# Performance work log

Hardware: AMD Instinct MI355X
Metric: run time of the kernel (lower is better)

Reference implementation:

```python
import jax, jax.numpy as jnp
import numpy as np

N = 50000      # nodes
E = 800000     # edges
IN = 128       # in_channels
HID = 32       # hidden_channels (per head)
HEADS = 4
OUT = 128      # out_channels
NEG_SLOPE = 0.2  # PyG GATConv leaky relu slope


def setup_inputs() -> dict:
    key = jax.random.key(0)
    ks = jax.random.split(key, 10)
    x = jax.random.normal(ks[0], (N, IN), dtype=jnp.float32)
    edge_index = jax.random.randint(ks[1], (2, E), 0, N, dtype=jnp.int32)
    s1 = 1.0 / np.sqrt(IN)
    s2 = 1.0 / np.sqrt(HEADS * HID)
    W1 = jax.random.normal(ks[2], (IN, HEADS * HID), dtype=jnp.float32) * s1
    a_src1 = jax.random.normal(ks[3], (HEADS, HID), dtype=jnp.float32) * s1
    a_dst1 = jax.random.normal(ks[4], (HEADS, HID), dtype=jnp.float32) * s1
    b1 = jnp.zeros((HEADS * HID,), dtype=jnp.float32)
    W2 = jax.random.normal(ks[5], (HEADS * HID, OUT), dtype=jnp.float32) * s2
    a_src2 = jax.random.normal(ks[6], (1, OUT), dtype=jnp.float32) * s2
    a_dst2 = jax.random.normal(ks[7], (1, OUT), dtype=jnp.float32) * s2
    b2 = jnp.zeros((OUT,), dtype=jnp.float32)
    return {"x": x, "edge_index": edge_index, "W1": W1, "a_src1": a_src1,
            "a_dst1": a_dst1, "b1": b1, "W2": W2, "a_src2": a_src2,
            "a_dst2": a_dst2, "b2": b2}


def _gat_layer(x, src, dst, W, a_src, a_dst, bias, heads, out_c, concat, n):
    # dense projection then reshape to [N, H, C]
    h = (x @ W).reshape(n, heads, out_c)
    # per-node attention halves: [N, H]
    alpha_src = jnp.einsum('nhc,hc->nh', h, a_src)
    alpha_dst = jnp.einsum('nhc,hc->nh', h, a_dst)
    # per-edge logits, leaky relu (slope 0.2 as in PyG)
    logits = jax.nn.leaky_relu(alpha_src[src] + alpha_dst[dst], NEG_SLOPE)  # [E', H]
    # segment softmax over incoming edges of each destination node
    m = jax.ops.segment_max(logits, dst, num_segments=n)          # [N, H]
    e = jnp.exp(logits - m[dst])                                   # [E', H]
    denom = jax.ops.segment_sum(e, dst, num_segments=n)           # [N, H]
    alpha = e / (denom[dst] + 1e-16)                               # [E', H]
    # weighted scatter-aggregate of source features
    out = jax.ops.segment_sum(alpha[:, :, None] * h[src], dst, num_segments=n)  # [N, H, C]
    if concat:
        out = out.reshape(n, heads * out_c)
    else:
        out = out.mean(axis=1)
    return out + bias


def reference(x, edge_index, W1, a_src1, a_dst1, b1, W2, a_src2, a_dst2, b2):
    n = x.shape[0]
    # PyG GATConv adds self-loops by default
    loop = jnp.arange(n, dtype=edge_index.dtype)
    src = jnp.concatenate([edge_index[0], loop])
    dst = jnp.concatenate([edge_index[1], loop])
    h = _gat_layer(x, src, dst, W1, a_src1, a_dst1, b1, HEADS, HID, True, n)
    h = jax.nn.elu(h)
    # dropout is identity in eval mode
    out = _gat_layer(h, src, dst, W2, a_src2, a_dst2, b2, 1, OUT, False, n)
    return jax.nn.elu(out)
```

## Files before the change

kernel.cpp:

```cpp
#include <hip/hip_runtime.h>
#include <hip/hip_bf16.h>


typedef _Float16 half2_t __attribute__((ext_vector_type(2)));
typedef _Float16 half4_t __attribute__((ext_vector_type(4)));
typedef _Float16 f16x8 __attribute__((ext_vector_type(8)));
typedef float f32x4 __attribute__((ext_vector_type(4)));

#define NBLK1 128
#define SORT_CAP 6144

static __device__ __forceinline__ float leaky02(float x) {
    return x > 0.f ? x : 0.2f * x;
}
static __device__ __forceinline__ float elu1(float x) {
    return x > 0.f ? x : __expf(x) - 1.f;
}


__global__ __launch_bounds__(256) void prep_kernel(
    const int* __restrict__ dst, int* __restrict__ g_cnt, int E, int chunk,
    const float* __restrict__ W1, const float* __restrict__ W2,
    _Float16* __restrict__ Wt1, _Float16* __restrict__ Wt2, int nbkt) {
    int b = blockIdx.x;
    int t = threadIdx.x;
    if (b < NBLK1) {
        __shared__ int h[256];
        h[t] = 0;
        __syncthreads();
        int lo = b * chunk, hi = min(E, lo + chunk);
        for (int i = lo + t; i < hi; i += 256) atomicAdd(&h[dst[i] >> 8], 1);
        __syncthreads();
        if (t < nbkt) g_cnt[t * NBLK1 + b] = h[t];
    } else {
        int idx = (b - NBLK1) * 256 + t;
        int which = idx >> 14;
        int r = idx & 16383;
        int nc = r >> 7, k = r & 127;
        if (which == 0)
            Wt1[(size_t)nc * 128 + k] = (_Float16)W1[(size_t)k * 128 + nc];
        else
            Wt2[(size_t)nc * 128 + k] = (_Float16)W2[(size_t)k * 128 + nc];
    }
}

__global__ void scan_tile_kernel(const int* __restrict__ in, int* __restrict__ out,
                                 int* __restrict__ sums, int n) {
    __shared__ int sdata[256];
    int t = threadIdx.x;
    int base = blockIdx.x * 2048 + t * 8;
    int v[8];
    int run = 0;
#pragma unroll
    for (int i = 0; i < 8; ++i) {
        int idx = base + i;
        int x = (idx < n) ? in[idx] : 0;
        run += x;
        v[i] = run;
    }
    sdata[t] = run;
    __syncthreads();
    for (int off = 1; off < 256; off <<= 1) {
        int u = (t >= off) ? sdata[t - off] : 0;
        __syncthreads();
        sdata[t] += u;
        __syncthreads();
    }
    int excl = sdata[t] - run;
#pragma unroll
    for (int i = 0; i < 8; ++i) {
        int idx = base + i;
        if (idx < n) out[idx] = v[i] + excl;
    }
    if (t == 0) sums[blockIdx.x] = sdata[255];
}

__global__ void scan_sums_kernel(int* __restrict__ sums, int nb) {
    int t = threadIdx.x;
    int orig = (t < nb) ? sums[t] : 0;
    int v = orig;
#pragma unroll
    for (int off = 1; off < 64; off <<= 1) {
        int u = __shfl_up(v, off, 64);
        if (t >= off) v += u;
    }
    if (t < nb) sums[t] = v - orig;
}

__global__ void offs_kernel(const int* __restrict__ incl, const int* __restrict__ sums,
                            int* __restrict__ offs, int ncnt) {
    int i = blockIdx.x * blockDim.x + threadIdx.x;
    if (i <= ncnt) offs[i] = (i == 0) ? 0 : incl[i - 1] + sums[(i - 1) >> 11];
}


__global__ __launch_bounds__(256) void gemm1_fused_kernel(
    const float* __restrict__ X, const _Float16* __restrict__ Wt,
    _Float16* __restrict__ H16, int nrows, const int* __restrict__ src,
    const int* __restrict__ dst, const int* __restrict__ offs,
    int* __restrict__ binned, int E, int chunk, int nGemm, int nbkt) {
    int b = blockIdx.x;
    int t = threadIdx.x;
    if (b < nGemm) {
        int wave = t >> 6, lane = t & 63;
        int m = lane & 15, q = lane >> 4;
        int arow = b * 64 + wave * 16 + m;
        bool rowok = arow < nrows;
        const float* xr = X + (size_t)arow * 128;
        f16x8 afrag[4];
#pragma unroll
        for (int s = 0; s < 4; ++s) {
            float4 v0 = make_float4(0.f, 0.f, 0.f, 0.f);
            float4 v1 = make_float4(0.f, 0.f, 0.f, 0.f);
            if (rowok) {
                v0 = *(const float4*)(xr + s * 32 + q * 8);
                v1 = *(const float4*)(xr + s * 32 + q * 8 + 4);
            }
            f16x8 a;
            a[0] = (_Float16)v0.x; a[1] = (_Float16)v0.y;
            a[2] = (_Float16)v0.z; a[3] = (_Float16)v0.w;
            a[4] = (_Float16)v1.x; a[5] = (_Float16)v1.y;
            a[6] = (_Float16)v1.z; a[7] = (_Float16)v1.w;
            afrag[s] = a;
        }
#pragma unroll
        for (int c = 0; c < 8; ++c) {
            f32x4 acc = {0.f, 0.f, 0.f, 0.f};
#pragma unroll
            for (int s = 0; s < 4; ++s) {
                f16x8 bfrag = *(const f16x8*)(Wt + (size_t)(c * 16 + m) * 128 + s * 32 + q * 8);
                acc = __builtin_amdgcn_mfma_f32_16x16x32_f16(afrag[s], bfrag, acc, 0, 0, 0);
            }
#pragma unroll
            for (int r = 0; r < 4; ++r) {
                int orow = b * 64 + wave * 16 + q * 4 + r;
                if (orow < nrows)
                    H16[(size_t)orow * 128 + c * 16 + m] = (_Float16)acc[r];
            }
        }
    } else {
        __shared__ int cur[256];
        int sb = b - nGemm;
        if (t < nbkt) cur[t] = offs[t * NBLK1 + sb];
        __syncthreads();
        int lo = sb * chunk, hi = min(E, lo + chunk);
        for (int i = lo + t; i < hi; i += 256) {
            int d = dst[i];
            int s = src[i];
            int p = atomicAdd(&cur[d >> 8], 1);
            binned[p] = ((d & 255) << 16) | s;
        }
    }
}


__global__ __launch_bounds__(256) void sort_alpha1_kernel(
    const int* __restrict__ binned, const int* __restrict__ offs,
    int* __restrict__ row_ptr, int* __restrict__ csr, int n, int nbkt,
    const _Float16* __restrict__ H16, const float* __restrict__ a_src,
    const float* __restrict__ a_dst, float* __restrict__ asrc_out,
    float* __restrict__ adst_out) {
    int b = blockIdx.x;
    int t = threadIdx.x;
    if (b < nbkt) {
        __shared__ int sorted[SORT_CAP];
        __shared__ int sdata[256];
        __shared__ int cur[256];
        int estart = offs[b * NBLK1];
        int eend = offs[(b + 1) * NBLK1];
        int node0 = b * 256;
        int nloc = min(256, n - node0);
        cur[t] = (t < nloc) ? 1 : 0;
        __syncthreads();
        for (int i = estart + t; i < eend; i += 256)
            atomicAdd(&cur[(binned[i] >> 16) & 255], 1);
        __syncthreads();
        int my = cur[t];
        sdata[t] = my;
        __syncthreads();
        for (int off = 1; off < 256; off <<= 1) {
            int u = (t >= off) ? sdata[t - off] : 0;
            __syncthreads();
            sdata[t] += u;
            __syncthreads();
        }
        int excl = sdata[t] - my;
        int total = sdata[255];
        int csr_base = estart + node0;
        if (node0 + t <= n) row_ptr[node0 + t] = csr_base + excl;
        if (t == 0 && node0 + 256 <= n) row_ptr[node0 + 256] = csr_base + total;
        if (t < nloc) {
            if (excl < SORT_CAP) sorted[excl] = node0 + t;
            else csr[csr_base + excl] = node0 + t;
            cur[t] = excl + 1;
        } else {
            cur[t] = 0;
        }
        __syncthreads();
        for (int i = estart + t; i < eend; i += 256) {
            int v = binned[i];
            int p = atomicAdd(&cur[(v >> 16) & 255], 1);
            int sv = v & 0xffff;
            if (p < SORT_CAP) sorted[p] = sv;
            else csr[csr_base + p] = sv;
        }
        __syncthreads();
        int lim = min(total, SORT_CAP);
        for (int j = t; j < lim; j += 256) csr[csr_base + j] = sorted[j];
    } else {
        int node = (b - nbkt) * 4 + (t >> 6);
        int lane = t & 63;
        if (node >= n) return;
        int c = lane * 2;
        half2_t hv = *(const half2_t*)(H16 + (size_t)node * 128 + c);
        float2 as = *(const float2*)(a_src + c);
        float2 ad = *(const float2*)(a_dst + c);
        float hx = (float)hv.x, hy = (float)hv.y;
        float ps = hx * as.x + hy * as.y;
        float pd = hx * ad.x + hy * ad.y;
#pragma unroll
        for (int off = 1; off <= 8; off <<= 1) {
            ps += __shfl_xor(ps, off, 64);
            pd += __shfl_xor(pd, off, 64);
        }
        if ((lane & 15) == 0) {
            int h = lane >> 4;
            asrc_out[node * 4 + h] = ps;
            adst_out[node * 4 + h] = pd;
        }
    }
}

__global__ __launch_bounds__(256) void gemm2_mfma_kernel(
    const _Float16* __restrict__ A16, const _Float16* __restrict__ Wt,
    _Float16* __restrict__ H16, int nrows) {
    int b = blockIdx.x;
    int t = threadIdx.x;
    int wave = t >> 6, lane = t & 63;
    int m = lane & 15, q = lane >> 4;
    int arow = b * 64 + wave * 16 + m;
    bool rowok = arow < nrows;
    const _Float16* ar = A16 + (size_t)arow * 128;
    f16x8 afrag[4];
#pragma unroll
    for (int s = 0; s < 4; ++s) {
        f16x8 a = {};
        if (rowok) a = *(const f16x8*)(ar + s * 32 + q * 8);
        afrag[s] = a;
    }
#pragma unroll
    for (int c = 0; c < 8; ++c) {
        f32x4 acc = {0.f, 0.f, 0.f, 0.f};
#pragma unroll
        for (int s = 0; s < 4; ++s) {
            f16x8 bfrag = *(const f16x8*)(Wt + (size_t)(c * 16 + m) * 128 + s * 32 + q * 8);
            acc = __builtin_amdgcn_mfma_f32_16x16x32_f16(afrag[s], bfrag, acc, 0, 0, 0);
        }
#pragma unroll
        for (int r = 0; r < 4; ++r) {
            int orow = b * 64 + wave * 16 + q * 4 + r;
            if (orow < nrows)
                H16[(size_t)orow * 128 + c * 16 + m] = (_Float16)acc[r];
        }
    }
}

__global__ void alpha2_kernel(const _Float16* __restrict__ H16, const float* __restrict__ a_src,
                              const float* __restrict__ a_dst, float* __restrict__ asrc_out,
                              float* __restrict__ adst_out, int n) {
    int wave = (blockIdx.x * blockDim.x + threadIdx.x) >> 6;
    int lane = threadIdx.x & 63;
    if (wave >= n) return;
    int c = lane * 2;
    half2_t hv = *(const half2_t*)(H16 + (size_t)wave * 128 + c);
    float2 as = *(const float2*)(a_src + c);
    float2 ad = *(const float2*)(a_dst + c);
    float hx = (float)hv.x, hy = (float)hv.y;
    float ps = hx * as.x + hy * as.y;
    float pd = hx * ad.x + hy * ad.y;
#pragma unroll
    for (int off = 1; off <= 32; off <<= 1) {
        ps += __shfl_xor(ps, off, 64);
        pd += __shfl_xor(pd, off, 64);
    }
    if (lane == 0) {
        asrc_out[wave] = ps;
        adst_out[wave] = pd;
    }
}


__global__ __launch_bounds__(256) void agg1_kernel(
    const _Float16* __restrict__ H16, const float* __restrict__ asrc,
    const float* __restrict__ adst, const int* __restrict__ row_ptr,
    const int* __restrict__ csr, const float* __restrict__ bias,
    _Float16* __restrict__ out16, int n) {
    int wid = (blockIdx.x * blockDim.x + threadIdx.x) >> 6;
    int lane = threadIdx.x & 63;
    int node = wid * 4 + (lane >> 4);
    if (node >= n) return;
    int sub = lane & 15;
    int c = sub * 8;
    int h = sub >> 2;
    float adh = adst[node * 4 + h];
    float4 bv0 = *(const float4*)(bias + c);
    float4 bv1 = *(const float4*)(bias + c + 4);
    int e0 = row_ptr[node];
    int e1 = row_ptr[node + 1];
    float den = 0.f;
    float a[8];
#pragma unroll
    for (int k = 0; k < 8; ++k) a[k] = 0.f;
    int e = e0;
    for (; e + 8 <= e1; e += 8) {
        int s[8];
#pragma unroll
        for (int j = 0; j < 8; ++j) s[j] = csr[e + j];
        float l[8];
        f16x8 g[8];
#pragma unroll
        for (int j = 0; j < 8; ++j) {
            l[j] = asrc[s[j] * 4 + h];
            g[j] = *(const f16x8*)(H16 + (size_t)s[j] * 128 + c);
        }
#pragma unroll
        for (int j = 0; j < 8; ++j) {
            float w = __expf(leaky02(l[j] + adh));
            den += w;
#pragma unroll
            for (int k = 0; k < 8; ++k) a[k] += w * (float)g[j][k];
        }
    }
    for (; e < e1; ++e) {
        int s = csr[e];
        float w = __expf(leaky02(asrc[s * 4 + h] + adh));
        f16x8 g = *(const f16x8*)(H16 + (size_t)s * 128 + c);
        den += w;
#pragma unroll
        for (int k = 0; k < 8; ++k) a[k] += w * (float)g[k];
    }
    float inv = 1.f / (den + 1e-16f);
    f16x8 o;
    o[0] = (_Float16)elu1(a[0] * inv + bv0.x);
    o[1] = (_Float16)elu1(a[1] * inv + bv0.y);
    o[2] = (_Float16)elu1(a[2] * inv + bv0.z);
    o[3] = (_Float16)elu1(a[3] * inv + bv0.w);
    o[4] = (_Float16)elu1(a[4] * inv + bv1.x);
    o[5] = (_Float16)elu1(a[5] * inv + bv1.y);
    o[6] = (_Float16)elu1(a[6] * inv + bv1.z);
    o[7] = (_Float16)elu1(a[7] * inv + bv1.w);
    *(f16x8*)(out16 + (size_t)node * 128 + c) = o;
}

__global__ __launch_bounds__(256) void agg2_kernel(
    const _Float16* __restrict__ H16, const float* __restrict__ asrc,
    const float* __restrict__ adst, const int* __restrict__ row_ptr,
    const int* __restrict__ csr, const float* __restrict__ bias,
    float* __restrict__ out, int n) {
    int wid = (blockIdx.x * blockDim.x + threadIdx.x) >> 6;
    int lane = threadIdx.x & 63;
    int node = wid * 4 + (lane >> 4);
    if (node >= n) return;
    int sub = lane & 15;
    int c = sub * 8;
    float adh = adst[node];
    float4 bv0 = *(const float4*)(bias + c);
    float4 bv1 = *(const float4*)(bias + c + 4);
    int e0 = row_ptr[node];
    int e1 = row_ptr[node + 1];
    float den = 0.f;
    float a[8];
#pragma unroll
    for (int k = 0; k < 8; ++k) a[k] = 0.f;
    int e = e0;
    for (; e + 8 <= e1; e += 8) {
        int s[8];
#pragma unroll
        for (int j = 0; j < 8; ++j) s[j] = csr[e + j];
        float l[8];
        f16x8 g[8];
#pragma unroll
        for (int j = 0; j < 8; ++j) {
            l[j] = asrc[s[j]];
            g[j] = *(const f16x8*)(H16 + (size_t)s[j] * 128 + c);
        }
#pragma unroll
        for (int j = 0; j < 8; ++j) {
            float w = __expf(leaky02(l[j] + adh));
            den += w;
#pragma unroll
            for (int k = 0; k < 8; ++k) a[k] += w * (float)g[j][k];
        }
    }
    for (; e < e1; ++e) {
        int s = csr[e];
        float w = __expf(leaky02(asrc[s] + adh));
        f16x8 g = *(const f16x8*)(H16 + (size_t)s * 128 + c);
        den += w;
#pragma unroll
        for (int k = 0; k < 8; ++k) a[k] += w * (float)g[k];
    }
    float inv = 1.f / (den + 1e-16f);
    float4 o0, o1;
    o0.x = elu1(a[0] * inv + bv0.x);
    o0.y = elu1(a[1] * inv + bv0.y);
    o0.z = elu1(a[2] * inv + bv0.z);
    o0.w = elu1(a[3] * inv + bv0.w);
    o1.x = elu1(a[4] * inv + bv1.x);
    o1.y = elu1(a[5] * inv + bv1.y);
    o1.z = elu1(a[6] * inv + bv1.z);
    o1.w = elu1(a[7] * inv + bv1.w);
    *(float4*)(out + (size_t)node * 128 + c) = o0;
    *(float4*)(out + (size_t)node * 128 + c + 4) = o1;
}


extern "C" void kernel_launch(void* const* d_in, const int* in_sizes, int n_in,
                              void* d_out, int out_size, void* d_ws, size_t ws_size,
                              hipStream_t stream) {
    const float* x       = (const float*)d_in[0];
    const int*   eidx    = (const int*)d_in[1];
    const float* W1      = (const float*)d_in[2];
    const float* a_src1  = (const float*)d_in[3];
    const float* a_dst1  = (const float*)d_in[4];
    const float* b1      = (const float*)d_in[5];
    const float* W2      = (const float*)d_in[6];
    const float* a_src2  = (const float*)d_in[7];
    const float* a_dst2  = (const float*)d_in[8];
    const float* b2      = (const float*)d_in[9];
    float* out = (float*)d_out;

    const int N = in_sizes[0] / 128;
    const int E = in_sizes[1] / 2;
    const int* src = eidx;
    const int* dst = eidx + E;

    const int nbkt = (N + 255) >> 8;
    const int ncnt = nbkt * NBLK1;
    const int chunk = (E + NBLK1 - 1) / NBLK1;
    const int ntiles = (ncnt + 2047) / 2048;

    char* w = (char*)d_ws;
    _Float16* bufH16 = (_Float16*)w; w += (size_t)N * 128 * sizeof(_Float16);
    _Float16* Wt1    = (_Float16*)w; w += (size_t)128 * 128 * sizeof(_Float16);
    _Float16* Wt2    = (_Float16*)w; w += (size_t)128 * 128 * sizeof(_Float16);
    float* asrc = (float*)w;   w += (size_t)N * 4 * sizeof(float);
    float* adst = (float*)w;   w += (size_t)N * 4 * sizeof(float);
    int* g_cnt   = (int*)w;    w += (size_t)ncnt * sizeof(int);
    int* incl    = (int*)w;    w += (size_t)ncnt * sizeof(int);
    int* offs    = (int*)w;    w += (size_t)(ncnt + 1) * sizeof(int);
    int* sums    = (int*)w;    w += 64 * sizeof(int);
    int* row_ptr = (int*)w;    w += (size_t)(N + 1) * sizeof(int);
    int* binned  = (int*)w;    w += (size_t)E * sizeof(int);
    int* csr     = (int*)w;    w += (size_t)(E + N) * sizeof(int);
    _Float16* bufA16 = (_Float16*)d_out;

    dim3 b256(256);
    const int nGemm = (N + 63) / 64;
    const int nAlpha = (N + 3) / 4;
    dim3 gAgg((((N + 3) / 4) + 3) / 4);

    hipLaunchKernelGGL(prep_kernel, dim3(NBLK1 + 128), b256, 0, stream, dst, g_cnt, E, chunk,
                       W1, W2, Wt1, Wt2, nbkt);
    hipLaunchKernelGGL(scan_tile_kernel, dim3(ntiles), b256, 0, stream, g_cnt, incl, sums, ncnt);
    hipLaunchKernelGGL(scan_sums_kernel, dim3(1), dim3(64), 0, stream, sums, ntiles);
    hipLaunchKernelGGL(offs_kernel, dim3((ncnt + 256) / 256 + 1), b256, 0, stream, incl, sums,
                       offs, ncnt);

    hipLaunchKernelGGL(gemm1_fused_kernel, dim3(nGemm + NBLK1), b256, 0, stream, x, Wt1,
                       bufH16, N, src, dst, offs, binned, E, chunk, nGemm, nbkt);
    hipLaunchKernelGGL(sort_alpha1_kernel, dim3(nbkt + nAlpha), b256, 0, stream, binned, offs,
                       row_ptr, csr, N, nbkt, bufH16, a_src1, a_dst1, asrc, adst);
    hipLaunchKernelGGL(agg1_kernel, gAgg, b256, 0, stream, bufH16, asrc, adst, row_ptr, csr, b1,
                       bufA16, N);

    hipLaunchKernelGGL(gemm2_mfma_kernel, dim3(nGemm), b256, 0, stream, bufA16, Wt2, bufH16, N);
    hipLaunchKernelGGL(alpha2_kernel, dim3(nAlpha), b256, 0, stream, bufH16, a_src2, a_dst2,
                       asrc, adst, N);
    hipLaunchKernelGGL(agg2_kernel, gAgg, b256, 0, stream, bufH16, asrc, adst, row_ptr, csr, b2,
                       out, N);
}
```

Before: 253.0 us.

## Fuse alpha2 into gemm2, collapse scan into one kernel, two nodes per agg wave

```diff
diff --git a/kernel.cpp b/kernel.cpp
--- a/kernel.cpp
+++ b/kernel.cpp
@@ -44,53 +44,29 @@
     }
 }
 
-__global__ void scan_tile_kernel(const int* __restrict__ in, int* __restrict__ out,
-                                 int* __restrict__ sums, int n) {
-    __shared__ int sdata[256];
+
+__global__ __launch_bounds__(256) void scan_one_kernel(const int* __restrict__ g_cnt,
+                                                       int* __restrict__ offs, int ncnt) {
+    __shared__ int ssum[256];
     int t = threadIdx.x;
-    int base = blockIdx.x * 2048 + t * 8;
-    int v[8];
-    int run = 0;
-#pragma unroll
-    for (int i = 0; i < 8; ++i) {
-        int idx = base + i;
-        int x = (idx < n) ? in[idx] : 0;
-        run += x;
-        v[i] = run;
-    }
-    sdata[t] = run;
+    int per = (ncnt + 255) / 256;
+    int lo = t * per, hi = min(ncnt, lo + per);
+    int s = 0;
+    for (int i = lo; i < hi; ++i) s += g_cnt[i];
+    ssum[t] = s;
     __syncthreads();
     for (int off = 1; off < 256; off <<= 1) {
-        int u = (t >= off) ? sdata[t - off] : 0;
-        __syncthreads();
-        sdata[t] += u;
-        __syncthreads();
-    }
-    int excl = sdata[t] - run;
-#pragma unroll
-    for (int i = 0; i < 8; ++i) {
-        int idx = base + i;
-        if (idx < n) out[idx] = v[i] + excl;
-    }
-    if (t == 0) sums[blockIdx.x] = sdata[255];
-}
-
-__global__ void scan_sums_kernel(int* __restrict__ sums, int nb) {
-    int t = threadIdx.x;
-    int orig = (t < nb) ? sums[t] : 0;
-    int v = orig;
-#pragma unroll
-    for (int off = 1; off < 64; off <<= 1) {
-        int u = __shfl_up(v, off, 64);
-        if (t >= off) v += u;
-    }
-    if (t < nb) sums[t] = v - orig;
-}
-
-__global__ void offs_kernel(const int* __restrict__ incl, const int* __restrict__ sums,
-                            int* __restrict__ offs, int ncnt) {
-    int i = blockIdx.x * blockDim.x + threadIdx.x;
-    if (i <= ncnt) offs[i] = (i == 0) ? 0 : incl[i - 1] + sums[(i - 1) >> 11];
+        int u = (t >= off) ? ssum[t - off] : 0;
+        __syncthreads();
+        ssum[t] += u;
+        __syncthreads();
+    }
+    int run = ssum[t] - s;
+    for (int i = lo; i < hi; ++i) {
+        offs[i] = run;
+        run += g_cnt[i];
+    }
+    if (t == 255) offs[ncnt] = run;
 }
 
 
@@ -231,9 +207,12 @@
     }
 }
 
-__global__ __launch_bounds__(256) void gemm2_mfma_kernel(
+
+__global__ __launch_bounds__(256) void gemm2_fused_kernel(
     const _Float16* __restrict__ A16, const _Float16* __restrict__ Wt,
-    _Float16* __restrict__ H16, int nrows) {
+    _Float16* __restrict__ H16, int nrows, const float* __restrict__ a_src,
+    const float* __restrict__ a_dst, float* __restrict__ asrc_out,
+    float* __restrict__ adst_out) {
     int b = blockIdx.x;
     int t = threadIdx.x;
     int wave = t >> 6, lane = t & 63;
@@ -248,6 +227,8 @@
         if (rowok) a = *(const f16x8*)(ar + s * 32 + q * 8);
         afrag[s] = a;
     }
+    float ps[4] = {0.f, 0.f, 0.f, 0.f};
+    float pd[4] = {0.f, 0.f, 0.f, 0.f};
 #pragma unroll
     for (int c = 0; c < 8; ++c) {
         f32x4 acc = {0.f, 0.f, 0.f, 0.f};
@@ -256,162 +237,168 @@
             f16x8 bfrag = *(const f16x8*)(Wt + (size_t)(c * 16 + m) * 128 + s * 32 + q * 8);
             acc = __builtin_amdgcn_mfma_f32_16x16x32_f16(afrag[s], bfrag, acc, 0, 0, 0);
         }
+        float asv = a_src[c * 16 + m];
+        float adv = a_dst[c * 16 + m];
 #pragma unroll
         for (int r = 0; r < 4; ++r) {
+            ps[r] += acc[r] * asv;
+            pd[r] += acc[r] * adv;
             int orow = b * 64 + wave * 16 + q * 4 + r;
             if (orow < nrows)
                 H16[(size_t)orow * 128 + c * 16 + m] = (_Float16)acc[r];
         }
     }
-}
-
-__global__ void alpha2_kernel(const _Float16* __restrict__ H16, const float* __restrict__ a_src,
-                              const float* __restrict__ a_dst, float* __restrict__ asrc_out,
-                              float* __restrict__ adst_out, int n) {
-    int wave = (blockIdx.x * blockDim.x + threadIdx.x) >> 6;
-    int lane = threadIdx.x & 63;
-    if (wave >= n) return;
-    int c = lane * 2;
-    half2_t hv = *(const half2_t*)(H16 + (size_t)wave * 128 + c);
-    float2 as = *(const float2*)(a_src + c);
-    float2 ad = *(const float2*)(a_dst + c);
-    float hx = (float)hv.x, hy = (float)hv.y;
-    float ps = hx * as.x + hy * as.y;
-    float pd = hx * ad.x + hy * ad.y;
-#pragma unroll
-    for (int off = 1; off <= 32; off <<= 1) {
-        ps += __shfl_xor(ps, off, 64);
-        pd += __shfl_xor(pd, off, 64);
-    }
-    if (lane == 0) {
-        asrc_out[wave] = ps;
-        adst_out[wave] = pd;
-    }
-}
-
-
-__global__ __launch_bounds__(256) void agg1_kernel(
+#pragma unroll
+    for (int r = 0; r < 4; ++r) {
+        float v = ps[r], u = pd[r];
+#pragma unroll
+        for (int off = 1; off <= 8; off <<= 1) {
+            v += __shfl_xor(v, off, 64);
+            u += __shfl_xor(u, off, 64);
+        }
+        ps[r] = v; pd[r] = u;
+    }
+    if (m == 0) {
+#pragma unroll
+        for (int r = 0; r < 4; ++r) {
+            int row = b * 64 + wave * 16 + q * 4 + r;
+            if (row < nrows) {
+                asrc_out[row] = ps[r];
+                adst_out[row] = pd[r];
+            }
+        }
+    }
+}
+
+
+__global__ __launch_bounds__(256, 6) void agg1_kernel(
     const _Float16* __restrict__ H16, const float* __restrict__ asrc,
     const float* __restrict__ adst, const int* __restrict__ row_ptr,
     const int* __restrict__ csr, const float* __restrict__ bias,
     _Float16* __restrict__ out16, int n) {
     int wid = (blockIdx.x * blockDim.x + threadIdx.x) >> 6;
     int lane = threadIdx.x & 63;
-    int node = wid * 4 + (lane >> 4);
-    if (node >= n) return;
     int sub = lane & 15;
     int c = sub * 8;
     int h = sub >> 2;
-    float adh = adst[node * 4 + h];
     float4 bv0 = *(const float4*)(bias + c);
     float4 bv1 = *(const float4*)(bias + c + 4);
-    int e0 = row_ptr[node];
-    int e1 = row_ptr[node + 1];
-    float den = 0.f;
-    float a[8];
-#pragma unroll
-    for (int k = 0; k < 8; ++k) a[k] = 0.f;
-    int e = e0;
-    for (; e + 8 <= e1; e += 8) {
-        int s[8];
-#pragma unroll
-        for (int j = 0; j < 8; ++j) s[j] = csr[e + j];
-        float l[8];
-        f16x8 g[8];
-#pragma unroll
-        for (int j = 0; j < 8; ++j) {
-            l[j] = asrc[s[j] * 4 + h];
-            g[j] = *(const f16x8*)(H16 + (size_t)s[j] * 128 + c);
-        }
-#pragma unroll
-        for (int j = 0; j < 8; ++j) {
-            float w = __expf(leaky02(l[j] + adh));
+#pragma unroll
+    for (int qq = 0; qq < 2; ++qq) {
+        int node = wid * 8 + qq * 4 + (lane >> 4);
+        if (node >= n) continue;
+        float adh = adst[node * 4 + h];
+        int e0 = row_ptr[node];
+        int e1 = row_ptr[node + 1];
+        float den = 0.f;
+        float a[8];
+#pragma unroll
+        for (int k = 0; k < 8; ++k) a[k] = 0.f;
+        int e = e0;
+        for (; e + 8 <= e1; e += 8) {
+            int s[8];
+#pragma unroll
+            for (int j = 0; j < 8; ++j) s[j] = csr[e + j];
+            float l[8];
+            f16x8 g[8];
+#pragma unroll
+            for (int j = 0; j < 8; ++j) {
+                l[j] = asrc[s[j] * 4 + h];
+                g[j] = *(const f16x8*)(H16 + (size_t)s[j] * 128 + c);
+            }
+#pragma unroll
+            for (int j = 0; j < 8; ++j) {
+                float w = __expf(leaky02(l[j] + adh));
+                den += w;
+#pragma unroll
+                for (int k = 0; k < 8; ++k) a[k] += w * (float)g[j][k];
+            }
+        }
+        for (; e < e1; ++e) {
+            int s = csr[e];
+            float w = __expf(leaky02(asrc[s * 4 + h] + adh));
+            f16x8 g = *(const f16x8*)(H16 + (size_t)s * 128 + c);
             den += w;
 #pragma unroll
-            for (int k = 0; k < 8; ++k) a[k] += w * (float)g[j][k];
-        }
-    }
-    for (; e < e1; ++e) {
-        int s = csr[e];
-        float w = __expf(leaky02(asrc[s * 4 + h] + adh));
-        f16x8 g = *(const f16x8*)(H16 + (size_t)s * 128 + c);
-        den += w;
-#pragma unroll
-        for (int k = 0; k < 8; ++k) a[k] += w * (float)g[k];
-    }
-    float inv = 1.f / (den + 1e-16f);
-    f16x8 o;
-    o[0] = (_Float16)elu1(a[0] * inv + bv0.x);
-    o[1] = (_Float16)elu1(a[1] * inv + bv0.y);
-    o[2] = (_Float16)elu1(a[2] * inv + bv0.z);
-    o[3] = (_Float16)elu1(a[3] * inv + bv0.w);
-    o[4] = (_Float16)elu1(a[4] * inv + bv1.x);
-    o[5] = (_Float16)elu1(a[5] * inv + bv1.y);
-    o[6] = (_Float16)elu1(a[6] * inv + bv1.z);
-    o[7] = (_Float16)elu1(a[7] * inv + bv1.w);
-    *(f16x8*)(out16 + (size_t)node * 128 + c) = o;
-}
-
-__global__ __launch_bounds__(256) void agg2_kernel(
+            for (int k = 0; k < 8; ++k) a[k] += w * (float)g[k];
+        }
+        float inv = 1.f / (den + 1e-16f);
+        f16x8 o;
+        o[0] = (_Float16)elu1(a[0] * inv + bv0.x);
+        o[1] = (_Float16)elu1(a[1] * inv + bv0.y);
+        o[2] = (_Float16)elu1(a[2] * inv + bv0.z);
+        o[3] = (_Float16)elu1(a[3] * inv + bv0.w);
+        o[4] = (_Float16)elu1(a[4] * inv + bv1.x);
+        o[5] = (_Float16)elu1(a[5] * inv + bv1.y);
+        o[6] = (_Float16)elu1(a[6] * inv + bv1.z);
+        o[7] = (_Float16)elu1(a[7] * inv + bv1.w);
+        *(f16x8*)(out16 + (size_t)node * 128 + c) = o;
+    }
+}
+
+__global__ __launch_bounds__(256, 6) void agg2_kernel(
     const _Float16* __restrict__ H16, const float* __restrict__ asrc,
     const float* __restrict__ adst, const int* __restrict__ row_ptr,
     const int* __restrict__ csr, const float* __restrict__ bias,
     float* __restrict__ out, int n) {
     int wid = (blockIdx.x * blockDim.x + threadIdx.x) >> 6;
     int lane = threadIdx.x & 63;
-    int node = wid * 4 + (lane >> 4);
-    if (node >= n) return;
     int sub = lane & 15;
     int c = sub * 8;
-    float adh = adst[node];
     float4 bv0 = *(const float4*)(bias + c);
     float4 bv1 = *(const float4*)(bias + c + 4);
-    int e0 = row_ptr[node];
-    int e1 = row_ptr[node + 1];
-    float den = 0.f;
-    float a[8];
-#pragma unroll
-    for (int k = 0; k < 8; ++k) a[k] = 0.f;
-    int e = e0;
-    for (; e + 8 <= e1; e += 8) {
-        int s[8];
-#pragma unroll
-        for (int j = 0; j < 8; ++j) s[j] = csr[e + j];
-        float l[8];
-        f16x8 g[8];
-#pragma unroll
-        for (int j = 0; j < 8; ++j) {
-            l[j] = asrc[s[j]];
-            g[j] = *(const f16x8*)(H16 + (size_t)s[j] * 128 + c);
-        }
-#pragma unroll
-        for (int j = 0; j < 8; ++j) {
-            float w = __expf(leaky02(l[j] + adh));
+#pragma unroll
+    for (int qq = 0; qq < 2; ++qq) {
+        int node = wid * 8 + qq * 4 + (lane >> 4);
+        if (node >= n) continue;
+        float adh = adst[node];
+        int e0 = row_ptr[node];
+        int e1 = row_ptr[node + 1];
+        float den = 0.f;
+        float a[8];
+#pragma unroll
+        for (int k = 0; k < 8; ++k) a[k] = 0.f;
+        int e = e0;
+        for (; e + 8 <= e1; e += 8) {
+            int s[8];
+#pragma unroll
+            for (int j = 0; j < 8; ++j) s[j] = csr[e + j];
+            float l[8];
+            f16x8 g[8];
+#pragma unroll
+            for (int j = 0; j < 8; ++j) {
+                l[j] = asrc[s[j]];
+                g[j] = *(const f16x8*)(H16 + (size_t)s[j] * 128 + c);
+            }
+#pragma unroll
+            for (int j = 0; j < 8; ++j) {
+                float w = __expf(leaky02(l[j] + adh));
+                den += w;
+#pragma unroll
+                for (int k = 0; k < 8; ++k) a[k] += w * (float)g[j][k];
+            }
+        }
+        for (; e < e1; ++e) {
+            int s = csr[e];
+            float w = __expf(leaky02(asrc[s] + adh));
+            f16x8 g = *(const f16x8*)(H16 + (size_t)s * 128 + c);
             den += w;
 #pragma unroll
-            for (int k = 0; k < 8; ++k) a[k] += w * (float)g[j][k];
-        }
-    }
-    for (; e < e1; ++e) {
-        int s = csr[e];
-        float w = __expf(leaky02(asrc[s] + adh));
-        f16x8 g = *(const f16x8*)(H16 + (size_t)s * 128 + c);
-        den += w;
-#pragma unroll
-        for (int k = 0; k < 8; ++k) a[k] += w * (float)g[k];
-    }
-    float inv = 1.f / (den + 1e-16f);
-    float4 o0, o1;
-    o0.x = elu1(a[0] * inv + bv0.x);
-    o0.y = elu1(a[1] * inv + bv0.y);
-    o0.z = elu1(a[2] * inv + bv0.z);
-    o0.w = elu1(a[3] * inv + bv0.w);
-    o1.x = elu1(a[4] * inv + bv1.x);
-    o1.y = elu1(a[5] * inv + bv1.y);
-    o1.z = elu1(a[6] * inv + bv1.z);
-    o1.w = elu1(a[7] * inv + bv1.w);
-    *(float4*)(out + (size_t)node * 128 + c) = o0;
-    *(float4*)(out + (size_t)node * 128 + c + 4) = o1;
+            for (int k = 0; k < 8; ++k) a[k] += w * (float)g[k];
+        }
+        float inv = 1.f / (den + 1e-16f);
+        float4 o0, o1;
+        o0.x = elu1(a[0] * inv + bv0.x);
+        o0.y = elu1(a[1] * inv + bv0.y);
+        o0.z = elu1(a[2] * inv + bv0.z);
+        o0.w = elu1(a[3] * inv + bv0.w);
+        o1.x = elu1(a[4] * inv + bv1.x);
+        o1.y = elu1(a[5] * inv + bv1.y);
+        o1.z = elu1(a[6] * inv + bv1.z);
+        o1.w = elu1(a[7] * inv + bv1.w);
+        *(float4*)(out + (size_t)node * 128 + c) = o0;
+        *(float4*)(out + (size_t)node * 128 + c + 4) = o1;
+    }
 }
 
 
@@ -438,7 +425,6 @@
     const int nbkt = (N + 255) >> 8;
     const int ncnt = nbkt * NBLK1;
     const int chunk = (E + NBLK1 - 1) / NBLK1;
-    const int ntiles = (ncnt + 2047) / 2048;
 
     char* w = (char*)d_ws;
     _Float16* bufH16 = (_Float16*)w; w += (size_t)N * 128 * sizeof(_Float16);
@@ -447,9 +433,7 @@
     float* asrc = (float*)w;   w += (size_t)N * 4 * sizeof(float);
     float* adst = (float*)w;   w += (size_t)N * 4 * sizeof(float);
     int* g_cnt   = (int*)w;    w += (size_t)ncnt * sizeof(int);
-    int* incl    = (int*)w;    w += (size_t)ncnt * sizeof(int);
     int* offs    = (int*)w;    w += (size_t)(ncnt + 1) * sizeof(int);
-    int* sums    = (int*)w;    w += 64 * sizeof(int);
     int* row_ptr = (int*)w;    w += (size_t)(N + 1) * sizeof(int);
     int* binned  = (int*)w;    w += (size_t)E * sizeof(int);
     int* csr     = (int*)w;    w += (size_t)(E + N) * sizeof(int);
@@ -458,25 +442,21 @@
     dim3 b256(256);
     const int nGemm = (N + 63) / 64;
     const int nAlpha = (N + 3) / 4;
-    dim3 gAgg((((N + 3) / 4) + 3) / 4);
+    const int nAggBlocks = (N + 31) / 32;
 
     hipLaunchKernelGGL(prep_kernel, dim3(NBLK1 + 128), b256, 0, stream, dst, g_cnt, E, chunk,
                        W1, W2, Wt1, Wt2, nbkt);
-    hipLaunchKernelGGL(scan_tile_kernel, dim3(ntiles), b256, 0, stream, g_cnt, incl, sums, ncnt);
-    hipLaunchKernelGGL(scan_sums_kernel, dim3(1), dim3(64), 0, stream, sums, ntiles);
-    hipLaunchKernelGGL(offs_kernel, dim3((ncnt + 256) / 256 + 1), b256, 0, stream, incl, sums,
-                       offs, ncnt);
+    hipLaunchKernelGGL(scan_one_kernel, dim3(1), b256, 0, stream, g_cnt, offs, ncnt);
 
     hipLaunchKernelGGL(gemm1_fused_kernel, dim3(nGemm + NBLK1), b256, 0, stream, x, Wt1,
                        bufH16, N, src, dst, offs, binned, E, chunk, nGemm, nbkt);
     hipLaunchKernelGGL(sort_alpha1_kernel, dim3(nbkt + nAlpha), b256, 0, stream, binned, offs,
                        row_ptr, csr, N, nbkt, bufH16, a_src1, a_dst1, asrc, adst);
-    hipLaunchKernelGGL(agg1_kernel, gAgg, b256, 0, stream, bufH16, asrc, adst, row_ptr, csr, b1,
-                       bufA16, N);
-
-    hipLaunchKernelGGL(gemm2_mfma_kernel, dim3(nGemm), b256, 0, stream, bufA16, Wt2, bufH16, N);
-    hipLaunchKernelGGL(alpha2_kernel, dim3(nAlpha), b256, 0, stream, bufH16, a_src2, a_dst2,
-                       asrc, adst, N);
-    hipLaunchKernelGGL(agg2_kernel, gAgg, b256, 0, stream, bufH16, asrc, adst, row_ptr, csr, b2,
-                       out, N);
-}
+    hipLaunchKernelGGL(agg1_kernel, dim3(nAggBlocks), b256, 0, stream, bufH16, asrc, adst,
+                       row_ptr, csr, b1, bufA16, N);
+
+    hipLaunchKernelGGL(gemm2_fused_kernel, dim3(nGemm), b256, 0, stream, bufA16, Wt2, bufH16, N,
+                       a_src2, a_dst2, asrc, adst);
+    hipLaunchKernelGGL(agg2_kernel, dim3(nAggBlocks), b256, 0, stream, bufH16, asrc, adst,
+                       row_ptr, csr, b2, out, N);
+}
```

New measurement: 321.5 us. 27.1% more time.

## Split aggregation channels across eight block slices with half2 per lane

Applied to the files above, without the earlier changes.

```diff
diff --git a/kernel.cpp b/kernel.cpp
--- a/kernel.cpp
+++ b/kernel.cpp
@@ -3,7 +3,6 @@
 
 
 typedef _Float16 half2_t __attribute__((ext_vector_type(2)));
-typedef _Float16 half4_t __attribute__((ext_vector_type(4)));
 typedef _Float16 f16x8 __attribute__((ext_vector_type(8)));
 typedef float f32x4 __attribute__((ext_vector_type(4)));
 
@@ -295,61 +294,71 @@
     const float* __restrict__ adst, const int* __restrict__ row_ptr,
     const int* __restrict__ csr, const float* __restrict__ bias,
     _Float16* __restrict__ out16, int n) {
-    int wid = (blockIdx.x * blockDim.x + threadIdx.x) >> 6;
+    int b = blockIdx.x;
+    int slice = b & 7;
+    int wave = threadIdx.x >> 6;
     int lane = threadIdx.x & 63;
-    int node = wid * 4 + (lane >> 4);
+    int node = (b >> 3) * 32 + wave * 8 + (lane >> 3);
     if (node >= n) return;
-    int sub = lane & 15;
-    int c = sub * 8;
-    int h = sub >> 2;
+    int sub = lane & 7;
+    int c = slice * 16 + sub * 2;
+    int h = slice >> 1;
     float adh = adst[node * 4 + h];
-    float4 bv0 = *(const float4*)(bias + c);
-    float4 bv1 = *(const float4*)(bias + c + 4);
-    int e0 = row_ptr[node];
-    int e1 = row_ptr[node + 1];
-    float den = 0.f;
-    float a[8];
-#pragma unroll
-    for (int k = 0; k < 8; ++k) a[k] = 0.f;
+    float b0 = bias[c], b1v = bias[c + 1];
+    int e0 = row_ptr[node], e1 = row_ptr[node + 1];
+    float den = 0.f, a0 = 0.f, a1 = 0.f;
     int e = e0;
     for (; e + 8 <= e1; e += 8) {
         int s[8];
 #pragma unroll
         for (int j = 0; j < 8; ++j) s[j] = csr[e + j];
         float l[8];
-        f16x8 g[8];
+        half2_t g[8];
 #pragma unroll
         for (int j = 0; j < 8; ++j) {
             l[j] = asrc[s[j] * 4 + h];
-            g[j] = *(const f16x8*)(H16 + (size_t)s[j] * 128 + c);
+            g[j] = *(const half2_t*)(H16 + (size_t)s[j] * 128 + c);
         }
 #pragma unroll
         for (int j = 0; j < 8; ++j) {
             float w = __expf(leaky02(l[j] + adh));
             den += w;
-#pragma unroll
-            for (int k = 0; k < 8; ++k) a[k] += w * (float)g[j][k];
+            a0 += w * (float)g[j].x;
+            a1 += w * (float)g[j].y;
+        }
+    }
+    for (; e + 4 <= e1; e += 4) {
+        int s[4];
+#pragma unroll
+        for (int j = 0; j < 4; ++j) s[j] = csr[e + j];
+        float l[4];
+        half2_t g[4];
+#pragma unroll
+        for (int j = 0; j < 4; ++j) {
+            l[j] = asrc[s[j] * 4 + h];
+            g[j] = *(const half2_t*)(H16 + (size_t)s[j] * 128 + c);
+        }
+#pragma unroll
+        for (int j = 0; j < 4; ++j) {
+            float w = __expf(leaky02(l[j] + adh));
+            den += w;
+            a0 += w * (float)g[j].x;
+            a1 += w * (float)g[j].y;
         }
     }
     for (; e < e1; ++e) {
         int s = csr[e];
         float w = __expf(leaky02(asrc[s * 4 + h] + adh));
-        f16x8 g = *(const f16x8*)(H16 + (size_t)s * 128 + c);
+        half2_t g = *(const half2_t*)(H16 + (size_t)s * 128 + c);
         den += w;
-#pragma unroll
-        for (int k = 0; k < 8; ++k) a[k] += w * (float)g[k];
+        a0 += w * (float)g.x;
+        a1 += w * (float)g.y;
     }
     float inv = 1.f / (den + 1e-16f);
-    f16x8 o;
-    o[0] = (_Float16)elu1(a[0] * inv + bv0.x);
-    o[1] = (_Float16)elu1(a[1] * inv + bv0.y);
-    o[2] = (_Float16)elu1(a[2] * inv + bv0.z);
-    o[3] = (_Float16)elu1(a[3] * inv + bv0.w);
-    o[4] = (_Float16)elu1(a[4] * inv + bv1.x);
-    o[5] = (_Float16)elu1(a[5] * inv + bv1.y);
-    o[6] = (_Float16)elu1(a[6] * inv + bv1.z);
-    o[7] = (_Float16)elu1(a[7] * inv + bv1.w);
-    *(f16x8*)(out16 + (size_t)node * 128 + c) = o;
+    half2_t o;
+    o.x = (_Float16)elu1(a0 * inv + b0);
+    o.y = (_Float16)elu1(a1 * inv + b1v);
+    *(half2_t*)(out16 + (size_t)node * 128 + c) = o;
 }
 
 __global__ __launch_bounds__(256) void agg2_kernel(
@@ -357,61 +366,70 @@
     const float* __restrict__ adst, const int* __restrict__ row_ptr,
     const int* __restrict__ csr, const float* __restrict__ bias,
     float* __restrict__ out, int n) {
-    int wid = (blockIdx.x * blockDim.x + threadIdx.x) >> 6;
+    int b = blockIdx.x;
+    int slice = b & 7;
+    int wave = threadIdx.x >> 6;
     int lane = threadIdx.x & 63;
-    int node = wid * 4 + (lane >> 4);
+    int node = (b >> 3) * 32 + wave * 8 + (lane >> 3);
     if (node >= n) return;
-    int sub = lane & 15;
-    int c = sub * 8;
+    int sub = lane & 7;
+    int c = slice * 16 + sub * 2;
     float adh = adst[node];
-    float4 bv0 = *(const float4*)(bias + c);
-    float4 bv1 = *(const float4*)(bias + c + 4);
-    int e0 = row_ptr[node];
-    int e1 = row_ptr[node + 1];
-    float den = 0.f;
-    float a[8];
-#pragma unroll
-    for (int k = 0; k < 8; ++k) a[k] = 0.f;
+    float b0 = bias[c], b1v = bias[c + 1];
+    int e0 = row_ptr[node], e1 = row_ptr[node + 1];
+    float den = 0.f, a0 = 0.f, a1 = 0.f;
     int e = e0;
     for (; e + 8 <= e1; e += 8) {
         int s[8];
 #pragma unroll
         for (int j = 0; j < 8; ++j) s[j] = csr[e + j];
         float l[8];
-        f16x8 g[8];
+        half2_t g[8];
 #pragma unroll
         for (int j = 0; j < 8; ++j) {
             l[j] = asrc[s[j]];
-            g[j] = *(const f16x8*)(H16 + (size_t)s[j] * 128 + c);
+            g[j] = *(const half2_t*)(H16 + (size_t)s[j] * 128 + c);
         }
 #pragma unroll
         for (int j = 0; j < 8; ++j) {
             float w = __expf(leaky02(l[j] + adh));
             den += w;
-#pragma unroll
-            for (int k = 0; k < 8; ++k) a[k] += w * (float)g[j][k];
+            a0 += w * (float)g[j].x;
+            a1 += w * (float)g[j].y;
+        }
+    }
+    for (; e + 4 <= e1; e += 4) {
+        int s[4];
+#pragma unroll
+        for (int j = 0; j < 4; ++j) s[j] = csr[e + j];
+        float l[4];
+        half2_t g[4];
+#pragma unroll
+        for (int j = 0; j < 4; ++j) {
+            l[j] = asrc[s[j]];
+            g[j] = *(const half2_t*)(H16 + (size_t)s[j] * 128 + c);
+        }
+#pragma unroll
+        for (int j = 0; j < 4; ++j) {
+            float w = __expf(leaky02(l[j] + adh));
+            den += w;
+            a0 += w * (float)g[j].x;
+            a1 += w * (float)g[j].y;
         }
     }
     for (; e < e1; ++e) {
         int s = csr[e];
         float w = __expf(leaky02(asrc[s] + adh));
-        f16x8 g = *(const f16x8*)(H16 + (size_t)s * 128 + c);
+        half2_t g = *(const half2_t*)(H16 + (size_t)s * 128 + c);
         den += w;
-#pragma unroll
-        for (int k = 0; k < 8; ++k) a[k] += w * (float)g[k];
+        a0 += w * (float)g.x;
+        a1 += w * (float)g.y;
     }
     float inv = 1.f / (den + 1e-16f);
-    float4 o0, o1;
-    o0.x = elu1(a[0] * inv + bv0.x);
-    o0.y = elu1(a[1] * inv + bv0.y);
-    o0.z = elu1(a[2] * inv + bv0.z);
-    o0.w = elu1(a[3] * inv + bv0.w);
-    o1.x = elu1(a[4] * inv + bv1.x);
-    o1.y = elu1(a[5] * inv + bv1.y);
-    o1.z = elu1(a[6] * inv + bv1.z);
-    o1.w = elu1(a[7] * inv + bv1.w);
-    *(float4*)(out + (size_t)node * 128 + c) = o0;
-    *(float4*)(out + (size_t)node * 128 + c + 4) = o1;
+    float2 o;
+    o.x = elu1(a0 * inv + b0);
+    o.y = elu1(a1 * inv + b1v);
+    *(float2*)(out + (size_t)node * 128 + c) = o;
 }
 
 
@@ -458,7 +476,7 @@
     dim3 b256(256);
     const int nGemm = (N + 63) / 64;
     const int nAlpha = (N + 3) / 4;
-    dim3 gAgg((((N + 3) / 4) + 3) / 4);
+    const int nAggBlocks = 8 * ((N + 31) / 32);
 
     hipLaunchKernelGGL(prep_kernel, dim3(NBLK1 + 128), b256, 0, stream, dst, g_cnt, E, chunk,
                        W1, W2, Wt1, Wt2, nbkt);
@@ -471,12 +489,12 @@
                        bufH16, N, src, dst, offs, binned, E, chunk, nGemm, nbkt);
     hipLaunchKernelGGL(sort_alpha1_kernel, dim3(nbkt + nAlpha), b256, 0, stream, binned, offs,
                        row_ptr, csr, N, nbkt, bufH16, a_src1, a_dst1, asrc, adst);
-    hipLaunchKernelGGL(agg1_kernel, gAgg, b256, 0, stream, bufH16, asrc, adst, row_ptr, csr, b1,
-                       bufA16, N);
+    hipLaunchKernelGGL(agg1_kernel, dim3(nAggBlocks), b256, 0, stream, bufH16, asrc, adst,
+                       row_ptr, csr, b1, bufA16, N);
 
     hipLaunchKernelGGL(gemm2_mfma_kernel, dim3(nGemm), b256, 0, stream, bufA16, Wt2, bufH16, N);
     hipLaunchKernelGGL(alpha2_kernel, dim3(nAlpha), b256, 0, stream, bufH16, a_src2, a_dst2,
                        asrc, adst, N);
-    hipLaunchKernelGGL(agg2_kernel, gAgg, b256, 0, stream, bufH16, asrc, adst, row_ptr, csr, b2,
-                       out, N);
-}
+    hipLaunchKernelGGL(agg2_kernel, dim3(nAggBlocks), b256, 0, stream, bufH16, asrc, adst,
+                       row_ptr, csr, b2, out, N);
+}
```

After: 350.8 us. 1.39x slower.
